# Performance work log

Hardware: AMD Instinct MI355X
Metric: run time of the kernel (lower is better)

Reference implementation:

```python
import jax, jax.numpy as jnp
import numpy as np

EPS = 1e-6
TEMP_GEO = 0.07
W_LOCAL = 0.5
W_SHARP = 0.5


def _l2norm(x):
    return x / jnp.clip(jnp.linalg.norm(x, axis=-1, keepdims=True), 1e-12)


def setup_inputs() -> dict:
    key = jax.random.key(0)
    ks = jax.random.split(key, 6)
    B, L, S, C = 8, 1024, 1024, 128
    N, P = 8, 256
    q_geo = _l2norm(jax.random.normal(ks[0], (B, L, C), jnp.float32))
    geo_pos = _l2norm(jax.random.normal(ks[1], (B, S, C), jnp.float32))
    label = jax.random.randint(ks[2], (B, L, S), 0, 2, jnp.int32)
    q_cl = jax.random.normal(ks[3], (N, P, C), jnp.float32)
    cl_pos = jax.random.normal(ks[4], (N, P, C), jnp.float32)
    idx = jax.random.randint(ks[5], (N,), 0, P, jnp.int32)
    return {"q_geo": q_geo, "q_cl": q_cl, "geo_pos": geo_pos,
            "cl_pos": cl_pos, "label": label, "idx": idx}


def _masked_mean(v, m):
    # per-sample mean over the [L,S] plane of entries where m is True
    m = m.astype(v.dtype)
    return jnp.sum(v * m, axis=(1, 2)) / jnp.maximum(jnp.sum(m, axis=(1, 2)), 1.0)


def _loftr_loss(conf, label):
    # standard LoFTR coarse CE loss (LoFTRLoss source absent from repo snippet)
    conf = jnp.clip(conf, EPS, 1.0 - EPS)
    pos = label == 1
    neg = label == 0
    pos_loss = _masked_mean(-jnp.log(conf), pos)          # [B]
    neg_loss = _masked_mean(-jnp.log(1.0 - conf), neg)    # [B]
    loss = pos_loss + neg_loss
    return jnp.mean(loss), jnp.mean(pos_loss), jnp.mean(neg_loss)


def _geometric_loss(q, k, label):
    sim = jnp.einsum('blc,bsc->bls', q, k) / TEMP_GEO        # [B,L,S]
    conf = jax.nn.softmax(sim, axis=1) * jax.nn.softmax(sim, axis=2)
    return _loftr_loss(conf, label)


def _sharpness_loss(q, k, label):
    sim = (1.0 + jnp.einsum('blc,bsc->bls', q, k)) / 2.0     # [B,L,S]
    # column stats (over L, dim=0 per sample) -> sharpness1 [B,S]
    s1 = (jnp.max(sim, axis=1) - jnp.mean(sim, axis=1)) / jnp.std(sim, axis=1, ddof=1)
    sharp1 = jax.nn.softmax(s1, axis=-1)
    # row stats (over S, dim=1 per sample) -> sharpness2 [B,L]
    s2 = (jnp.max(sim, axis=2) - jnp.mean(sim, axis=2)) / jnp.std(sim, axis=2, ddof=1)
    sharp2 = jax.nn.softmax(s2, axis=-1)
    simc = jnp.clip(sim, EPS, 1.0 - EPS)
    nll = -jnp.log(simc)
    pos = (label == 1).astype(simc.dtype)
    neg = (label == 0)
    loss1 = jnp.sum(nll * sharp1[:, None, :] * pos, axis=(1, 2))   # [B]
    loss2 = jnp.sum(nll * sharp2[:, :, None] * pos, axis=(1, 2))   # [B]
    loss3 = _masked_mean(-jnp.log(1.0 - simc), neg)                # [B]
    losses = (loss1 + loss2) / 2.0 + loss3
    return sharp1, jnp.mean(losses)


def _contrast_loss(q, all_k):
    # intended math of GeCoContrast: full cosine matrix, diag positives, tail negatives
    N = q.shape[0]
    sim = (1.0 + _l2norm(q) @ _l2norm(all_k).T) / 2.0   # [N, M]
    sim = jnp.clip(sim, EPS, 1.0 - EPS)
    l_pos = jnp.diagonal(sim[:, :N])                    # [N]
    l_neg = sim[:, N:]                                  # [N, M-N]
    return (jnp.mean(-jnp.log(l_pos)) + jnp.mean(-jnp.log(1.0 - l_neg))) / 2.0


def _forward(q_geo, q_cl, geo_pos, cl_pos, label, idx):
    loss_geo, geo_pos_loss, geo_neg_loss = _geometric_loss(q_geo, geo_pos, label)
    sharpness, loss_sharp = _sharpness_loss(q_geo, geo_pos, label)
    loss_geo = ((1.0 - W_SHARP) * loss_geo + W_SHARP * loss_sharp) * W_LOCAL

    N, P, C = q_cl.shape
    ar = jnp.arange(N)
    q_sel = q_cl[ar, idx]                               # [N,C]
    sel = cl_pos[ar, idx]                               # [N,C] positives moved to slot 0
    first = cl_pos[:, 0, :]
    swapped = cl_pos.at[ar, idx].set(first).at[:, 0, :].set(sel)
    cl_pos_save = sel
    all_k = jnp.concatenate([swapped[:, 0, :],
                             swapped[:, 1:, :].reshape(N * (P - 1), C)], axis=0)
    loss_cl = _contrast_loss(q_sel, all_k) * (1.0 - W_LOCAL)

    total = loss_geo + loss_cl
    return (sharpness, cl_pos_save, total, geo_pos_loss, geo_neg_loss, loss_sharp, loss_cl)


def reference(q_geo, q_cl, geo_pos, cl_pos, label, idx):
    return _forward(q_geo, q_cl, geo_pos, cl_pos, label, idx)
```

## Files before the change

kernel.cpp:

```cpp
#include <hip/hip_runtime.h>
#include <math.h>

#define BB 8
#define LL 1024
#define SS 1024
#define CC 128
#define NN 8
#define PP 256

static constexpr float EPS       = 1e-6f;
static constexpr float ONE_M_EPS = 1.0f - 1e-6f;
static constexpr float INV_T     = 1.0f / 0.07f;
static constexpr float NLL_MAX   = 13.815511f;
static constexpr float NLL_MIN   = 1.0000005e-6f;

static constexpr size_t DOTSZ      = (size_t)BB * LL * SS;
static constexpr size_t OFF_LSER   = DOTSZ;
static constexpr size_t OFF_S2RAW  = DOTSZ + 8192;
static constexpr size_t OFF_LSEC   = DOTSZ + 16384;
static constexpr size_t OFF_S1RAW  = DOTSZ + 24576;
static constexpr size_t OFF_SHARP2 = DOTSZ + 32768;
static constexpr size_t OFF_RP     = DOTSZ + 40960;
static constexpr size_t OFF_CP     = OFF_RP + 524288;
static constexpr size_t OFF_ACC    = OFF_CP + 524288;
static constexpr size_t OFF_ACCCL  = OFF_ACC + 48;
static constexpr size_t OFF_QN     = OFF_ACC + 64;

static constexpr int OUT_CLSAVE = 8192;
static constexpr int OUT_SCAL   = 9216;

typedef __bf16 bf16x8 __attribute__((ext_vector_type(8)));
typedef float  floatx4 __attribute__((ext_vector_type(4)));

__device__ __forceinline__ bf16x8 mkfrag(unsigned a, unsigned b, unsigned c, unsigned d) {
    uint4 t = make_uint4(a, b, c, d);
    return __builtin_bit_cast(bf16x8, t);
}

__device__ __forceinline__ void split_f4(float4 x,
                                         unsigned& hp0, unsigned& hp1,
                                         unsigned& lp0, unsigned& lp1) {
    unsigned u0 = __builtin_bit_cast(unsigned, x.x);
    unsigned u1 = __builtin_bit_cast(unsigned, x.y);
    unsigned u2 = __builtin_bit_cast(unsigned, x.z);
    unsigned u3 = __builtin_bit_cast(unsigned, x.w);
    unsigned r0 = u0 + 0x7FFFu + ((u0 >> 16) & 1u);
    unsigned r1 = u1 + 0x7FFFu + ((u1 >> 16) & 1u);
    unsigned r2 = u2 + 0x7FFFu + ((u2 >> 16) & 1u);
    unsigned r3 = u3 + 0x7FFFu + ((u3 >> 16) & 1u);
    float s0 = x.x - __builtin_bit_cast(float, r0 & 0xFFFF0000u);
    float s1 = x.y - __builtin_bit_cast(float, r1 & 0xFFFF0000u);
    float s2 = x.z - __builtin_bit_cast(float, r2 & 0xFFFF0000u);
    float s3 = x.w - __builtin_bit_cast(float, r3 & 0xFFFF0000u);
    hp0 = __builtin_amdgcn_perm(r1, r0, 0x07060302u);
    hp1 = __builtin_amdgcn_perm(r3, r2, 0x07060302u);
    lp0 = __builtin_amdgcn_perm(__builtin_bit_cast(unsigned, s1),
                                __builtin_bit_cast(unsigned, s0), 0x07060302u);
    lp1 = __builtin_amdgcn_perm(__builtin_bit_cast(unsigned, s3),
                                __builtin_bit_cast(unsigned, s2), 0x07060302u);
}

__global__ __launch_bounds__(512) void prep(const float* __restrict__ q_cl,
                                            const float* __restrict__ cl_pos,
                                            const int* __restrict__ idx,
                                            float* __restrict__ out, float* __restrict__ ws) {
    int tid = threadIdx.x;
    if (tid < 50) ws[OFF_ACC + tid] = 0.0f;
    int n = tid >> 6, lane = tid & 63;
    int in = idx[n];
    const float* q = q_cl + ((size_t)(n * PP + in)) * CC;
    float2 qv = *(const float2*)(q + 2 * lane);
    float ss = qv.x * qv.x + qv.y * qv.y;
    for (int o = 32; o; o >>= 1) ss += __shfl_xor(ss, o);
    float inv = 1.0f / fmaxf(sqrtf(ss), 1e-12f);
    *(float2*)(ws + OFF_QN + n * 128 + 2 * lane) = make_float2(qv.x * inv, qv.y * inv);
    const float* cp = cl_pos + ((size_t)(n * PP + in)) * CC;
    float2 cv = *(const float2*)(cp + 2 * lane);
    *(float2*)(out + OUT_CLSAVE + n * 128 + 2 * lane) = cv;
}

__global__ __launch_bounds__(256) void gemm_dot(const float* __restrict__ A,
                                                const float* __restrict__ Bm,
                                                float* __restrict__ dot,
                                                float* __restrict__ ws) {
    int tid  = threadIdx.x;
    int lane = tid & 63;
    int w    = tid >> 6;
    int t    = blockIdx.x * 4 + w;
    int b    = t >> 8;
    int rem  = t & 255;
    int lt   = rem >> 4, st = rem & 15;
    int l0   = lt * 64, s0 = st * 64;
    int fl   = lane & 15;
    int quad = lane >> 4;

    const float* Ab = A  + ((size_t)b * LL + l0) * CC;
    const float* Bb = Bm + ((size_t)b * SS + s0) * CC;

    floatx4 acc[4][4];
#pragma unroll
    for (int i = 0; i < 4; i++)
#pragma unroll
        for (int j = 0; j < 4; j++) acc[i][j] = (floatx4){0.f, 0.f, 0.f, 0.f};

    for (int c0 = 0; c0 < 128; c0 += 32) {
        float4 ax[4][2], bx[4][2];
#pragma unroll
        for (int mt = 0; mt < 4; mt++) {
            const float* p = Ab + (size_t)(mt * 16 + fl) * CC + c0 + quad * 8;
            ax[mt][0] = *(const float4*)p;
            ax[mt][1] = *(const float4*)(p + 4);
        }
#pragma unroll
        for (int nt = 0; nt < 4; nt++) {
            const float* p = Bb + (size_t)(nt * 16 + fl) * CC + c0 + quad * 8;
            bx[nt][0] = *(const float4*)p;
            bx[nt][1] = *(const float4*)(p + 4);
        }
        bf16x8 ah[4], al[4];
#pragma unroll
        for (int mt = 0; mt < 4; mt++) {
            unsigned h0, h1, h2, h3, q0, q1, q2, q3;
            split_f4(ax[mt][0], h0, h1, q0, q1);
            split_f4(ax[mt][1], h2, h3, q2, q3);
            ah[mt] = mkfrag(h0, h1, h2, h3);
            al[mt] = mkfrag(q0, q1, q2, q3);
        }
#pragma unroll
        for (int nt = 0; nt < 4; nt++) {
            unsigned h0, h1, h2, h3, q0, q1, q2, q3;
            split_f4(bx[nt][0], h0, h1, q0, q1);
            split_f4(bx[nt][1], h2, h3, q2, q3);
            bf16x8 bh = mkfrag(h0, h1, h2, h3);
            bf16x8 bl = mkfrag(q0, q1, q2, q3);
#pragma unroll
            for (int mt = 0; mt < 4; mt++) {
                acc[mt][nt] = __builtin_amdgcn_mfma_f32_16x16x32_bf16(ah[mt], bh, acc[mt][nt], 0, 0, 0);
                acc[mt][nt] = __builtin_amdgcn_mfma_f32_16x16x32_bf16(ah[mt], bl, acc[mt][nt], 0, 0, 0);
                acc[mt][nt] = __builtin_amdgcn_mfma_f32_16x16x32_bf16(al[mt], bh, acc[mt][nt], 0, 0, 0);
            }
        }
    }

    float* D = dot + ((size_t)b * LL + l0) * SS + s0;
#pragma unroll
    for (int mt = 0; mt < 4; mt++)
#pragma unroll
        for (int nt = 0; nt < 4; nt++) {
            int col = nt * 16 + fl;
#pragma unroll
            for (int r = 0; r < 4; r++) {
                int row = mt * 16 + quad * 4 + r;
                D[(size_t)row * SS + col] = acc[mt][nt][r];
            }
        }

    float ces[4], cmx[4], csm[4], csq[4];
#pragma unroll
    for (int nt = 0; nt < 4; nt++) { ces[nt] = 0.f; cmx[nt] = -1e30f; csm[nt] = 0.f; csq[nt] = 0.f; }
#pragma unroll
    for (int mt = 0; mt < 4; mt++) {
#pragma unroll
        for (int r = 0; r < 4; r++) {
            float es = 0.f, mx = -1e30f, sm = 0.f, sq = 0.f;
#pragma unroll
            for (int nt = 0; nt < 4; nt++) {
                float d  = acc[mt][nt][r];
                float e  = __expf(d * INV_T);
                float s2 = fmaf(0.5f, d, 0.5f);
                es += e; mx = fmaxf(mx, s2); sm += s2; sq += s2 * s2;
                ces[nt] += e; cmx[nt] = fmaxf(cmx[nt], s2); csm[nt] += s2; csq[nt] += s2 * s2;
            }
            for (int o = 1; o < 16; o <<= 1) {
                es += __shfl_xor(es, o);
                mx = fmaxf(mx, __shfl_xor(mx, o));
                sm += __shfl_xor(sm, o);
                sq += __shfl_xor(sq, o);
            }
            if (fl == 0) {
                int row = l0 + mt * 16 + quad * 4 + r;
                *(float4*)(ws + OFF_RP + (((size_t)(b * 16 + st)) * 1024 + row) * 4) =
                    make_float4(es, mx, sm, sq);
            }
        }
    }
#pragma unroll
    for (int nt = 0; nt < 4; nt++) {
        float es = ces[nt], mx = cmx[nt], sm = csm[nt], sq = csq[nt];
        for (int o = 16; o < 64; o <<= 1) {
            es += __shfl_xor(es, o);
            mx = fmaxf(mx, __shfl_xor(mx, o));
            sm += __shfl_xor(sm, o);
            sq += __shfl_xor(sq, o);
        }
        if (quad == 0) {
            int col = s0 + nt * 16 + fl;
            *(float4*)(ws + OFF_CP + (((size_t)(b * 16 + lt)) * 1024 + col) * 4) =
                make_float4(es, mx, sm, sq);
        }
    }
}

__global__ __launch_bounds__(256) void rc_combine(float* __restrict__ ws) {
    int g = (blockIdx.x & 31) * 256 + threadIdx.x;
    bool docol = blockIdx.x >= 32;
    int b = g >> 10, i = g & 1023;
    const float* part = ws + (docol ? OFF_CP : OFF_RP);
    float es = 0.f, mx = -1e30f, sm = 0.f, sq = 0.f;
#pragma unroll
    for (int t = 0; t < 16; t++) {
        float4 v = *(const float4*)(part + (((size_t)(b * 16 + t)) * 1024 + i) * 4);
        es += v.x; mx = fmaxf(mx, v.y); sm += v.z; sq += v.w;
    }
    float mean = sm * (1.0f / 1024.0f);
    float var  = (sq - sm * sm * (1.0f / 1024.0f)) * (1.0f / 1023.0f);
    float zs   = (mx - mean) / sqrtf(fmaxf(var, 1e-30f));
    if (!docol) {
        ws[OFF_LSER + g]  = __logf(es);
        ws[OFF_S2RAW + g] = zs;
    } else {
        ws[OFF_LSEC + g]  = __logf(es);
        ws[OFF_S1RAW + g] = zs;
    }
}

__global__ __launch_bounds__(256) void softmax16(float* __restrict__ ws, float* __restrict__ out) {
    int q = blockIdx.x;
    int b = q & 7;
    const float* src = ws + ((q < 8) ? OFF_S1RAW : OFF_S2RAW) + (size_t)b * 1024;
    float* dst = (q < 8) ? (out + (size_t)b * 1024) : (ws + OFF_SHARP2 + (size_t)b * 1024);
    float4 v = ((const float4*)src)[threadIdx.x];
    int lane = threadIdx.x & 63, wid = threadIdx.x >> 6;
    __shared__ float sb[4];
    __shared__ float red;
    float mx = fmaxf(fmaxf(v.x, v.y), fmaxf(v.z, v.w));
    for (int o = 32; o; o >>= 1) mx = fmaxf(mx, __shfl_xor(mx, o));
    if (!lane) sb[wid] = mx;
    __syncthreads();
    if (threadIdx.x == 0) red = fmaxf(fmaxf(sb[0], sb[1]), fmaxf(sb[2], sb[3]));
    __syncthreads();
    mx = red;
    float e0 = __expf(v.x - mx), e1 = __expf(v.y - mx), e2 = __expf(v.z - mx), e3 = __expf(v.w - mx);
    float sm = e0 + e1 + e2 + e3;
    for (int o = 32; o; o >>= 1) sm += __shfl_xor(sm, o);
    __syncthreads();
    if (!lane) sb[wid] = sm;
    __syncthreads();
    if (threadIdx.x == 0) red = sb[0] + sb[1] + sb[2] + sb[3];
    __syncthreads();
    float inv = 1.0f / red;
    ((float4*)dst)[threadIdx.x] = make_float4(e0 * inv, e1 * inv, e2 * inv, e3 * inv);
}

__device__ __forceinline__ void proc_elem(float d, int lab, float lcj, float sh1j,
                                          float lr, float s2v,
                                          float& posg, float& negg, float& l1, float& l2,
                                          float& negs, float& pcf) {
    float t = lr + lcj - d * (2.0f * INV_T);
    float isPos = (lab == 1) ? 1.0f : 0.0f;
    float isNeg = 1.0f - isPos;
    float tp   = fminf(fmaxf(t, NLL_MIN), NLL_MAX);
    float simc = fminf(fmaxf(fmaf(0.5f, d, 0.5f), EPS), ONE_M_EPS);
    float om   = fminf(fmaxf(fmaf(-0.5f, d, 0.5f), EPS), ONE_M_EPS);
    float nll2 = -__logf(simc);
    float cf   = fminf(fmaxf(__expf(-t), EPS), ONE_M_EPS);
    float nllg = -__logf(1.0f - cf);
    float nlls = -__logf(om);
    posg += isPos * tp;
    l1   += isPos * nll2 * sh1j;
    l2   += isPos * nll2 * s2v;
    pcf  += isPos;
    negg += isNeg * nllg;
    negs += isNeg * nlls;
}

__global__ __launch_bounds__(256) void main_loss(const float* __restrict__ dot,
                                                 const int* __restrict__ label,
                                                 const float* __restrict__ sharp1,
                                                 float* __restrict__ ws) {
    int b = blockIdx.y;
    int l0 = blockIdx.x * 4;
    int s = threadIdx.x * 4;
    float4 lc4 = *(const float4*)(ws + OFF_LSEC + (size_t)b * 1024 + s);
    float4 sh1 = *(const float4*)(sharp1 + (size_t)b * 1024 + s);
    const float* lser = ws + OFF_LSER + (size_t)b * 1024;
    const float* sh2  = ws + OFF_SHARP2 + (size_t)b * 1024;
    float posg = 0, negg = 0, l1 = 0, l2 = 0, negs = 0, pcf = 0;
#pragma unroll
    for (int r = 0; r < 4; r++) {
        int l = l0 + r;
        float lr  = lser[l];
        float s2v = sh2[l];
        size_t base = ((size_t)(b * 1024 + l)) * 1024 + s;
        float4 d4 = *(const float4*)(dot + base);
        int4  lb  = *(const int4*)(label + base);
        proc_elem(d4.x, lb.x, lc4.x, sh1.x, lr, s2v, posg, negg, l1, l2, negs, pcf);
        proc_elem(d4.y, lb.y, lc4.y, sh1.y, lr, s2v, posg, negg, l1, l2, negs, pcf);
        proc_elem(d4.z, lb.z, lc4.z, sh1.z, lr, s2v, posg, negg, l1, l2, negs, pcf);
        proc_elem(d4.w, lb.w, lc4.w, sh1.w, lr, s2v, posg, negg, l1, l2, negs, pcf);
    }
    float vals[6] = {posg, negg, l1, l2, negs, pcf};
    __shared__ float sb[6][4];
    int lane = threadIdx.x & 63, wid = threadIdx.x >> 6;
#pragma unroll
    for (int k = 0; k < 6; k++) {
        float v = vals[k];
        for (int o = 32; o; o >>= 1) v += __shfl_xor(v, o);
        if (!lane) sb[k][wid] = v;
    }
    __syncthreads();
    if (threadIdx.x < 6) {
        float r = sb[threadIdx.x][0] + sb[threadIdx.x][1] + sb[threadIdx.x][2] + sb[threadIdx.x][3];
        atomicAdd(ws + OFF_ACC + (size_t)b * 6 + threadIdx.x, r);
    }
}

__global__ __launch_bounds__(256) void contrast(const float* __restrict__ cl_pos,
                                                const int* __restrict__ idx,
                                                float* __restrict__ ws) {
    int j = blockIdx.x * 4 + (threadIdx.x >> 6);
    int lane = threadIdx.x & 63;
    int m, p;
    if (j < NN) {
        m = j; p = idx[j];
    } else {
        int jj = j - NN;
        m = jj / (PP - 1);
        p = 1 + (jj - m * (PP - 1));
        if (p == idx[m]) p = 0;
    }
    const float* k = cl_pos + ((size_t)(m * PP + p)) * CC;
    float2 kv = *(const float2*)(k + 2 * lane);
    float ksq = kv.x * kv.x + kv.y * kv.y;
    for (int o = 32; o; o >>= 1) ksq += __shfl_xor(ksq, o);
    float invkn = 1.0f / fmaxf(sqrtf(ksq), 1e-12f);
    float pos = 0.0f, neg = 0.0f;
    if (j < NN) {
        const float2 qv = *(const float2*)(ws + OFF_QN + j * 128 + 2 * lane);
        float dt = qv.x * kv.x + qv.y * kv.y;
        for (int o = 32; o; o >>= 1) dt += __shfl_xor(dt, o);
        float sim = fminf(fmaxf(fmaf(0.5f * invkn, dt, 0.5f), EPS), ONE_M_EPS);
        pos = -__logf(sim);
    } else {
#pragma unroll
        for (int n = 0; n < NN; n++) {
            const float2 qv = *(const float2*)(ws + OFF_QN + n * 128 + 2 * lane);
            float dt = qv.x * kv.x + qv.y * kv.y;
            for (int o = 32; o; o >>= 1) dt += __shfl_xor(dt, o);
            float om = fminf(fmaxf(fmaf(-0.5f * invkn, dt, 0.5f), EPS), ONE_M_EPS);
            neg -= __logf(om);
        }
    }
    __shared__ float sb[2][4];
    int w = threadIdx.x >> 6;
    if (!lane) { sb[0][w] = pos; sb[1][w] = neg; }
    __syncthreads();
    if (threadIdx.x == 0) {
        float ps = sb[0][0] + sb[0][1] + sb[0][2] + sb[0][3];
        float ng = sb[1][0] + sb[1][1] + sb[1][2] + sb[1][3];
        if (ps != 0.0f) atomicAdd(ws + OFF_ACCCL + 0, ps);
        if (ng != 0.0f) atomicAdd(ws + OFF_ACCCL + 1, ng);
    }
}

__global__ void finalize(float* __restrict__ out, const float* __restrict__ ws) {
    if (threadIdx.x != 0) return;
    float gp = 0, gn = 0, lsh = 0;
    for (int b = 0; b < 8; b++) {
        const float* a = ws + OFF_ACC + (size_t)b * 6;
        float pc = a[5];
        float nc = (float)((size_t)LL * SS) - pc;
        gp += a[0] / fmaxf(pc, 1.0f);
        gn += a[1] / fmaxf(nc, 1.0f);
        lsh += (a[2] + a[3]) * 0.5f + a[4] / fmaxf(nc, 1.0f);
    }
    gp *= 0.125f; gn *= 0.125f; lsh *= 0.125f;
    float lgeo = gp + gn;
    float lgw = (0.5f * lgeo + 0.5f * lsh) * 0.5f;
    float clp = ws[OFF_ACCCL + 0] / 8.0f;
    float cln = ws[OFF_ACCCL + 1] / (8.0f * 2040.0f);
    float lcl = (clp + cln) * 0.5f * 0.5f;
    out[OUT_SCAL + 0] = lgw + lcl;
    out[OUT_SCAL + 1] = gp;
    out[OUT_SCAL + 2] = gn;
    out[OUT_SCAL + 3] = lsh;
    out[OUT_SCAL + 4] = lcl;
}

extern "C" void kernel_launch(void* const* d_in, const int* in_sizes, int n_in,
                              void* d_out, int out_size, void* d_ws, size_t ws_size,
                              hipStream_t stream) {
    const float* q_geo   = (const float*)d_in[0];
    const float* q_cl    = (const float*)d_in[1];
    const float* geo_pos = (const float*)d_in[2];
    const float* cl_pos  = (const float*)d_in[3];
    const int*   label   = (const int*)d_in[4];
    const int*   idx     = (const int*)d_in[5];
    float* out = (float*)d_out;
    float* ws  = (float*)d_ws;
    float* dot = ws;

    prep<<<dim3(1), dim3(512), 0, stream>>>(q_cl, cl_pos, idx, out, ws);
    gemm_dot<<<dim3(512), dim3(256), 0, stream>>>(q_geo, geo_pos, dot, ws);
    rc_combine<<<dim3(64), dim3(256), 0, stream>>>(ws);
    softmax16<<<dim3(16), dim3(256), 0, stream>>>(ws, out);
    main_loss<<<dim3(256, 8), dim3(256), 0, stream>>>(dot, label, out, ws);
    contrast<<<dim3(512), dim3(256), 0, stream>>>(cl_pos, idx, ws);
    finalize<<<dim3(1), dim3(64), 0, stream>>>(out, ws);
}
```

Baseline: 165.1 us.

## Fuse small kernels into three launches with last-block finalize in main_loss

Folds the prep work into an extra block of the GEMM kernel, and merges the row/column combine with the sharpness softmax into one 'mid' kernel that also runs the contrastive loss blocks. The finalize step moves into main_loss using a global done-counter so the last block computes the scalar outputs. This cuts the pipeline from seven launches to three, removing launch gaps and the intermediate raw-sharpness round trip. It adds a threadfence and atomic counter to every main_loss block, and the counter must be zeroed each call, which relies on the prep block clearing it.

```diff
diff --git a/kernel.cpp b/kernel.cpp
--- a/kernel.cpp
+++ b/kernel.cpp
@@ -16,14 +16,13 @@
 
 static constexpr size_t DOTSZ      = (size_t)BB * LL * SS;
 static constexpr size_t OFF_LSER   = DOTSZ;
-static constexpr size_t OFF_S2RAW  = DOTSZ + 8192;
 static constexpr size_t OFF_LSEC   = DOTSZ + 16384;
-static constexpr size_t OFF_S1RAW  = DOTSZ + 24576;
 static constexpr size_t OFF_SHARP2 = DOTSZ + 32768;
 static constexpr size_t OFF_RP     = DOTSZ + 40960;
 static constexpr size_t OFF_CP     = OFF_RP + 524288;
 static constexpr size_t OFF_ACC    = OFF_CP + 524288;
 static constexpr size_t OFF_ACCCL  = OFF_ACC + 48;
+static constexpr size_t OFF_CNT    = OFF_ACC + 50;
 static constexpr size_t OFF_QN     = OFF_ACC + 64;
 
 static constexpr int OUT_CLSAVE = 8192;
@@ -60,32 +59,35 @@
                                 __builtin_bit_cast(unsigned, s2), 0x07060302u);
 }
 
-__global__ __launch_bounds__(512) void prep(const float* __restrict__ q_cl,
-                                            const float* __restrict__ cl_pos,
-                                            const int* __restrict__ idx,
-                                            float* __restrict__ out, float* __restrict__ ws) {
-    int tid = threadIdx.x;
-    if (tid < 50) ws[OFF_ACC + tid] = 0.0f;
-    int n = tid >> 6, lane = tid & 63;
-    int in = idx[n];
-    const float* q = q_cl + ((size_t)(n * PP + in)) * CC;
-    float2 qv = *(const float2*)(q + 2 * lane);
-    float ss = qv.x * qv.x + qv.y * qv.y;
-    for (int o = 32; o; o >>= 1) ss += __shfl_xor(ss, o);
-    float inv = 1.0f / fmaxf(sqrtf(ss), 1e-12f);
-    *(float2*)(ws + OFF_QN + n * 128 + 2 * lane) = make_float2(qv.x * inv, qv.y * inv);
-    const float* cp = cl_pos + ((size_t)(n * PP + in)) * CC;
-    float2 cv = *(const float2*)(cp + 2 * lane);
-    *(float2*)(out + OUT_CLSAVE + n * 128 + 2 * lane) = cv;
-}
-
 __global__ __launch_bounds__(256) void gemm_dot(const float* __restrict__ A,
                                                 const float* __restrict__ Bm,
+                                                const float* __restrict__ q_cl,
+                                                const float* __restrict__ cl_pos,
+                                                const int* __restrict__ idx,
+                                                float* __restrict__ out,
                                                 float* __restrict__ dot,
                                                 float* __restrict__ ws) {
     int tid  = threadIdx.x;
     int lane = tid & 63;
     int w    = tid >> 6;
+
+    if (blockIdx.x == 512) {
+        if (tid < 52) ws[OFF_ACC + tid] = 0.0f;
+        for (int n = w; n < NN; n += 4) {
+            int in = idx[n];
+            const float* q = q_cl + ((size_t)(n * PP + in)) * CC;
+            float2 qv = *(const float2*)(q + 2 * lane);
+            float ss = qv.x * qv.x + qv.y * qv.y;
+            for (int o = 32; o; o >>= 1) ss += __shfl_xor(ss, o);
+            float inv = 1.0f / fmaxf(sqrtf(ss), 1e-12f);
+            *(float2*)(ws + OFF_QN + n * 128 + 2 * lane) = make_float2(qv.x * inv, qv.y * inv);
+            const float* cp = cl_pos + ((size_t)(n * PP + in)) * CC;
+            float2 cv = *(const float2*)(cp + 2 * lane);
+            *(float2*)(out + OUT_CLSAVE + n * 128 + 2 * lane) = cv;
+        }
+        return;
+    }
+
     int t    = blockIdx.x * 4 + w;
     int b    = t >> 8;
     int rem  = t & 255;
@@ -201,55 +203,101 @@
     }
 }
 
-__global__ __launch_bounds__(256) void rc_combine(float* __restrict__ ws) {
-    int g = (blockIdx.x & 31) * 256 + threadIdx.x;
-    bool docol = blockIdx.x >= 32;
-    int b = g >> 10, i = g & 1023;
-    const float* part = ws + (docol ? OFF_CP : OFF_RP);
-    float es = 0.f, mx = -1e30f, sm = 0.f, sq = 0.f;
-#pragma unroll
-    for (int t = 0; t < 16; t++) {
-        float4 v = *(const float4*)(part + (((size_t)(b * 16 + t)) * 1024 + i) * 4);
-        es += v.x; mx = fmaxf(mx, v.y); sm += v.z; sq += v.w;
-    }
-    float mean = sm * (1.0f / 1024.0f);
-    float var  = (sq - sm * sm * (1.0f / 1024.0f)) * (1.0f / 1023.0f);
-    float zs   = (mx - mean) / sqrtf(fmaxf(var, 1e-30f));
-    if (!docol) {
-        ws[OFF_LSER + g]  = __logf(es);
-        ws[OFF_S2RAW + g] = zs;
+__global__ __launch_bounds__(256) void mid(const float* __restrict__ cl_pos,
+                                           const int* __restrict__ idx,
+                                           float* __restrict__ ws,
+                                           float* __restrict__ out) {
+    int q   = blockIdx.x;
+    int tid = threadIdx.x;
+    int lane = tid & 63, wid = tid >> 6;
+
+    if (q < 16) {
+        bool docol = (q < 8);
+        int b = q & 7;
+        const float* part = ws + (docol ? OFF_CP : OFF_RP) + (size_t)b * 16 * 1024 * 4;
+        float* lse = ws + (docol ? OFF_LSEC : OFF_LSER) + (size_t)b * 1024;
+        float zs[4];
+        float mxall = -1e30f;
+#pragma unroll
+        for (int r = 0; r < 4; r++) {
+            int i = tid + r * 256;
+            float es = 0.f, mx = -1e30f, sm = 0.f, sq = 0.f;
+#pragma unroll
+            for (int t = 0; t < 16; t++) {
+                float4 v = *(const float4*)(part + ((size_t)t * 1024 + i) * 4);
+                es += v.x; mx = fmaxf(mx, v.y); sm += v.z; sq += v.w;
+            }
+            float mean = sm * (1.0f / 1024.0f);
+            float var  = (sq - sm * sm * (1.0f / 1024.0f)) * (1.0f / 1023.0f);
+            zs[r] = (mx - mean) / sqrtf(fmaxf(var, 1e-30f));
+            mxall = fmaxf(mxall, zs[r]);
+            lse[i] = __logf(es);
+        }
+        __shared__ float sb[4];
+        __shared__ float red;
+        float mx = mxall;
+        for (int o = 32; o; o >>= 1) mx = fmaxf(mx, __shfl_xor(mx, o));
+        if (!lane) sb[wid] = mx;
+        __syncthreads();
+        if (tid == 0) red = fmaxf(fmaxf(sb[0], sb[1]), fmaxf(sb[2], sb[3]));
+        __syncthreads();
+        mx = red;
+        float e[4]; float smv = 0.f;
+#pragma unroll
+        for (int r = 0; r < 4; r++) { e[r] = __expf(zs[r] - mx); smv += e[r]; }
+        for (int o = 32; o; o >>= 1) smv += __shfl_xor(smv, o);
+        __syncthreads();
+        if (!lane) sb[wid] = smv;
+        __syncthreads();
+        if (tid == 0) red = sb[0] + sb[1] + sb[2] + sb[3];
+        __syncthreads();
+        float inv = 1.0f / red;
+        float* dst = docol ? (out + (size_t)b * 1024) : (ws + OFF_SHARP2 + (size_t)b * 1024);
+#pragma unroll
+        for (int r = 0; r < 4; r++) dst[tid + r * 256] = e[r] * inv;
     } else {
-        ws[OFF_LSEC + g]  = __logf(es);
-        ws[OFF_S1RAW + g] = zs;
-    }
-}
-
-__global__ __launch_bounds__(256) void softmax16(float* __restrict__ ws, float* __restrict__ out) {
-    int q = blockIdx.x;
-    int b = q & 7;
-    const float* src = ws + ((q < 8) ? OFF_S1RAW : OFF_S2RAW) + (size_t)b * 1024;
-    float* dst = (q < 8) ? (out + (size_t)b * 1024) : (ws + OFF_SHARP2 + (size_t)b * 1024);
-    float4 v = ((const float4*)src)[threadIdx.x];
-    int lane = threadIdx.x & 63, wid = threadIdx.x >> 6;
-    __shared__ float sb[4];
-    __shared__ float red;
-    float mx = fmaxf(fmaxf(v.x, v.y), fmaxf(v.z, v.w));
-    for (int o = 32; o; o >>= 1) mx = fmaxf(mx, __shfl_xor(mx, o));
-    if (!lane) sb[wid] = mx;
-    __syncthreads();
-    if (threadIdx.x == 0) red = fmaxf(fmaxf(sb[0], sb[1]), fmaxf(sb[2], sb[3]));
-    __syncthreads();
-    mx = red;
-    float e0 = __expf(v.x - mx), e1 = __expf(v.y - mx), e2 = __expf(v.z - mx), e3 = __expf(v.w - mx);
-    float sm = e0 + e1 + e2 + e3;
-    for (int o = 32; o; o >>= 1) sm += __shfl_xor(sm, o);
-    __syncthreads();
-    if (!lane) sb[wid] = sm;
-    __syncthreads();
-    if (threadIdx.x == 0) red = sb[0] + sb[1] + sb[2] + sb[3];
-    __syncthreads();
-    float inv = 1.0f / red;
-    ((float4*)dst)[threadIdx.x] = make_float4(e0 * inv, e1 * inv, e2 * inv, e3 * inv);
+        int j = (q - 16) * 4 + wid;
+        int m, p;
+        if (j < NN) {
+            m = j; p = idx[j];
+        } else {
+            int jj = j - NN;
+            m = jj / (PP - 1);
+            p = 1 + (jj - m * (PP - 1));
+            if (p == idx[m]) p = 0;
+        }
+        const float* k = cl_pos + ((size_t)(m * PP + p)) * CC;
+        float2 kv = *(const float2*)(k + 2 * lane);
+        float ksq = kv.x * kv.x + kv.y * kv.y;
+        for (int o = 32; o; o >>= 1) ksq += __shfl_xor(ksq, o);
+        float invkn = 1.0f / fmaxf(sqrtf(ksq), 1e-12f);
+        float pos = 0.0f, neg = 0.0f;
+        if (j < NN) {
+            const float2 qv = *(const float2*)(ws + OFF_QN + j * 128 + 2 * lane);
+            float dt = qv.x * kv.x + qv.y * kv.y;
+            for (int o = 32; o; o >>= 1) dt += __shfl_xor(dt, o);
+            float sim = fminf(fmaxf(fmaf(0.5f * invkn, dt, 0.5f), EPS), ONE_M_EPS);
+            pos = -__logf(sim);
+        } else {
+#pragma unroll
+            for (int n = 0; n < NN; n++) {
+                const float2 qv = *(const float2*)(ws + OFF_QN + n * 128 + 2 * lane);
+                float dt = qv.x * kv.x + qv.y * kv.y;
+                for (int o = 32; o; o >>= 1) dt += __shfl_xor(dt, o);
+                float om = fminf(fmaxf(fmaf(-0.5f * invkn, dt, 0.5f), EPS), ONE_M_EPS);
+                neg -= __logf(om);
+            }
+        }
+        __shared__ float cb[2][4];
+        if (!lane) { cb[0][wid] = pos; cb[1][wid] = neg; }
+        __syncthreads();
+        if (tid == 0) {
+            float ps = cb[0][0] + cb[0][1] + cb[0][2] + cb[0][3];
+            float ng = cb[1][0] + cb[1][1] + cb[1][2] + cb[1][3];
+            if (ps != 0.0f) atomicAdd(ws + OFF_ACCCL + 0, ps);
+            if (ng != 0.0f) atomicAdd(ws + OFF_ACCCL + 1, ng);
+        }
+    }
 }
 
 __device__ __forceinline__ void proc_elem(float d, int lab, float lcj, float sh1j,
@@ -274,10 +322,15 @@
     negs += isNeg * nlls;
 }
 
+__device__ __forceinline__ float coh_load(const float* p) {
+    return __hip_atomic_load(p, __ATOMIC_RELAXED, __HIP_MEMORY_SCOPE_AGENT);
+}
+
 __global__ __launch_bounds__(256) void main_loss(const float* __restrict__ dot,
                                                  const int* __restrict__ label,
                                                  const float* __restrict__ sharp1,
-                                                 float* __restrict__ ws) {
+                                                 float* __restrict__ ws,
+                                                 float* __restrict__ out) {
     int b = blockIdx.y;
     int l0 = blockIdx.x * 4;
     int s = threadIdx.x * 4;
@@ -313,78 +366,35 @@
         float r = sb[threadIdx.x][0] + sb[threadIdx.x][1] + sb[threadIdx.x][2] + sb[threadIdx.x][3];
         atomicAdd(ws + OFF_ACC + (size_t)b * 6 + threadIdx.x, r);
     }
-}
-
-__global__ __launch_bounds__(256) void contrast(const float* __restrict__ cl_pos,
-                                                const int* __restrict__ idx,
-                                                float* __restrict__ ws) {
-    int j = blockIdx.x * 4 + (threadIdx.x >> 6);
-    int lane = threadIdx.x & 63;
-    int m, p;
-    if (j < NN) {
-        m = j; p = idx[j];
-    } else {
-        int jj = j - NN;
-        m = jj / (PP - 1);
-        p = 1 + (jj - m * (PP - 1));
-        if (p == idx[m]) p = 0;
-    }
-    const float* k = cl_pos + ((size_t)(m * PP + p)) * CC;
-    float2 kv = *(const float2*)(k + 2 * lane);
-    float ksq = kv.x * kv.x + kv.y * kv.y;
-    for (int o = 32; o; o >>= 1) ksq += __shfl_xor(ksq, o);
-    float invkn = 1.0f / fmaxf(sqrtf(ksq), 1e-12f);
-    float pos = 0.0f, neg = 0.0f;
-    if (j < NN) {
-        const float2 qv = *(const float2*)(ws + OFF_QN + j * 128 + 2 * lane);
-        float dt = qv.x * kv.x + qv.y * kv.y;
-        for (int o = 32; o; o >>= 1) dt += __shfl_xor(dt, o);
-        float sim = fminf(fmaxf(fmaf(0.5f * invkn, dt, 0.5f), EPS), ONE_M_EPS);
-        pos = -__logf(sim);
-    } else {
-#pragma unroll
-        for (int n = 0; n < NN; n++) {
-            const float2 qv = *(const float2*)(ws + OFF_QN + n * 128 + 2 * lane);
-            float dt = qv.x * kv.x + qv.y * kv.y;
-            for (int o = 32; o; o >>= 1) dt += __shfl_xor(dt, o);
-            float om = fminf(fmaxf(fmaf(-0.5f * invkn, dt, 0.5f), EPS), ONE_M_EPS);
-            neg -= __logf(om);
-        }
-    }
-    __shared__ float sb[2][4];
-    int w = threadIdx.x >> 6;
-    if (!lane) { sb[0][w] = pos; sb[1][w] = neg; }
+    __threadfence();
     __syncthreads();
     if (threadIdx.x == 0) {
-        float ps = sb[0][0] + sb[0][1] + sb[0][2] + sb[0][3];
-        float ng = sb[1][0] + sb[1][1] + sb[1][2] + sb[1][3];
-        if (ps != 0.0f) atomicAdd(ws + OFF_ACCCL + 0, ps);
-        if (ng != 0.0f) atomicAdd(ws + OFF_ACCCL + 1, ng);
-    }
-}
-
-__global__ void finalize(float* __restrict__ out, const float* __restrict__ ws) {
-    if (threadIdx.x != 0) return;
-    float gp = 0, gn = 0, lsh = 0;
-    for (int b = 0; b < 8; b++) {
-        const float* a = ws + OFF_ACC + (size_t)b * 6;
-        float pc = a[5];
-        float nc = (float)((size_t)LL * SS) - pc;
-        gp += a[0] / fmaxf(pc, 1.0f);
-        gn += a[1] / fmaxf(nc, 1.0f);
-        lsh += (a[2] + a[3]) * 0.5f + a[4] / fmaxf(nc, 1.0f);
-    }
-    gp *= 0.125f; gn *= 0.125f; lsh *= 0.125f;
-    float lgeo = gp + gn;
-    float lgw = (0.5f * lgeo + 0.5f * lsh) * 0.5f;
-    float clp = ws[OFF_ACCCL + 0] / 8.0f;
-    float cln = ws[OFF_ACCCL + 1] / (8.0f * 2040.0f);
-    float lcl = (clp + cln) * 0.5f * 0.5f;
-    out[OUT_SCAL + 0] = lgw + lcl;
-    out[OUT_SCAL + 1] = gp;
-    out[OUT_SCAL + 2] = gn;
-    out[OUT_SCAL + 3] = lsh;
-    out[OUT_SCAL + 4] = lcl;
+        unsigned done = atomicAdd((unsigned*)(ws + OFF_CNT), 1u);
+        if (done == 2047u) {
+            __threadfence();
+            float gp = 0, gn = 0, lsh = 0;
+            for (int b2 = 0; b2 < 8; b2++) {
+                const float* a = ws + OFF_ACC + (size_t)b2 * 6;
+                float a0 = coh_load(a + 0), a1 = coh_load(a + 1), a2 = coh_load(a + 2);
+                float a3 = coh_load(a + 3), a4 = coh_load(a + 4), pc = coh_load(a + 5);
+                float nc = (float)((size_t)LL * SS) - pc;
+                gp += a0 / fmaxf(pc, 1.0f);
+                gn += a1 / fmaxf(nc, 1.0f);
+                lsh += (a2 + a3) * 0.5f + a4 / fmaxf(nc, 1.0f);
+            }
+            gp *= 0.125f; gn *= 0.125f; lsh *= 0.125f;
+            float lgeo = gp + gn;
+            float lgw = (0.5f * lgeo + 0.5f * lsh) * 0.5f;
+            float clp = coh_load(ws + OFF_ACCCL + 0) / 8.0f;
+            float cln = coh_load(ws + OFF_ACCCL + 1) / (8.0f * 2040.0f);
+            float lcl = (clp + cln) * 0.5f * 0.5f;
+            out[OUT_SCAL + 0] = lgw + lcl;
+            out[OUT_SCAL + 1] = gp;
+            out[OUT_SCAL + 2] = gn;
+            out[OUT_SCAL + 3] = lsh;
+            out[OUT_SCAL + 4] = lcl;
+        }
+    }
 }
 
 extern "C" void kernel_launch(void* const* d_in, const int* in_sizes, int n_in,
@@ -400,11 +410,7 @@
     float* ws  = (float*)d_ws;
     float* dot = ws;
 
-    prep<<<dim3(1), dim3(512), 0, stream>>>(q_cl, cl_pos, idx, out, ws);
-    gemm_dot<<<dim3(512), dim3(256), 0, stream>>>(q_geo, geo_pos, dot, ws);
-    rc_combine<<<dim3(64), dim3(256), 0, stream>>>(ws);
-    softmax16<<<dim3(16), dim3(256), 0, stream>>>(ws, out);
-    main_loss<<<dim3(256, 8), dim3(256), 0, stream>>>(dot, label, out, ws);
-    contrast<<<dim3(512), dim3(256), 0, stream>>>(cl_pos, idx, ws);
-    finalize<<<dim3(1), dim3(64), 0, stream>>>(out, ws);
-}
+    gemm_dot<<<dim3(513), dim3(256), 0, stream>>>(q_geo, geo_pos, q_cl, cl_pos, idx, out, dot, ws);
+    mid<<<dim3(528), dim3(256), 0, stream>>>(cl_pos, idx, ws, out);
+    main_loss<<<dim3(256, 8), dim3(256), 0, stream>>>(dot, label, out, ws, out);
+}
```

Measured after the change: 285.1 us. +72.7%, slower.
